# Performance work log

Measured on AMD Instinct MI355X. Metric: run time of the kernel, lower is better.

The kernel has to match this reference:

```python
import jax, jax.numpy as jnp
import numpy as np

B, C, H, W, K = 2, 64, 192, 192, 7
PAD = K // 2
EPS = 1e-6


def _win_idx(L):
    # NATTEN border handling: window is shifted (not zero-padded) to stay in-bounds.
    i = jnp.arange(L)
    start = jnp.clip(i - PAD, 0, L - K)            # [L] window start per query pos
    win = start[:, None] + jnp.arange(K)[None]     # [L,K] absolute key positions
    pb = (K - 1) - (i - start)                     # [L] rpb start index per query pos
    pbi = pb[:, None] + jnp.arange(K)[None]        # [L,K] rpb table indices
    return win, pbi


def setup_inputs() -> dict:
    key = jax.random.key(0)
    ks = jax.random.split(key, 10)
    g = jax.random.normal(ks[0], (B, C, H, W), jnp.float32)
    cd = jax.random.uniform(ks[1], (B, 1, H, W), dtype=jnp.float32)
    dense = jax.random.uniform(ks[2], (B, 1, H, W), dtype=jnp.float32)
    sel = jax.random.uniform(ks[3], (B, 1, H, W)) < 0.05
    sd = jnp.where(sel, dense, 0.0)
    mask = (jax.random.uniform(ks[4], (B, 1, H, W)) < 0.5).astype(jnp.float32)
    ln_w = 1.0 + 0.02 * jax.random.normal(ks[5], (C,), jnp.float32)
    ln_b = 0.02 * jax.random.normal(ks[6], (C,), jnp.float32)
    conv_w = 0.05 * jax.random.normal(ks[7], (2 * C, C + 1), jnp.float32)  # 1x1 conv
    conv_b = 0.02 * jax.random.normal(ks[8], (2 * C,), jnp.float32)
    rpb = 0.02 * jax.random.normal(ks[9], (1, 2 * K - 1, 2 * K - 1), jnp.float32)
    return {"g": g, "cd": cd, "sd": sd, "mask": mask,
            "ln_w": ln_w, "ln_b": ln_b, "conv_w": conv_w, "conv_b": conv_b, "rpb": rpb}


def reference(g, cd, sd, mask, ln_w, ln_b, conv_w, conv_b, rpb):
    # LayerNorm2d: normalize over channel dim per spatial location
    mu = g.mean(axis=1, keepdims=True)
    var = ((g - mu) ** 2).mean(axis=1, keepdims=True)
    gn = (g - mu) * jax.lax.rsqrt(var + EPS)
    gn = gn * ln_w[None, :, None, None] + ln_b[None, :, None, None]

    z = jnp.concatenate([gn, cd], axis=1)                      # [B,C+1,H,W]
    qk = jnp.einsum('bchw,oc->bohw', z, conv_w) + conv_b[None, :, None, None]
    q, k = qk[:, :C], qk[:, C:]
    k = k * mask

    qc = q.transpose(0, 2, 3, 1)                               # [B,H,W,C] single head
    kc = k.transpose(0, 2, 3, 1)
    rwin, rpbi = _win_idx(H)
    cwin, cpbi = _win_idx(W)

    # NATTEN qk + relative position bias over 7x7 neighborhoods
    k_win = kc[:, rwin][:, :, :, cwin]                         # [B,H,K,W,K,C]
    attn = jnp.einsum('bhwc,bhiwjc->bhwij', qc, k_win)         # [B,H,W,K,K]
    bias = rpb[0][rpbi][:, :, cpbi]                            # [H,K,W,K]
    attn = attn + bias.transpose(0, 2, 1, 3)[None]
    a = jax.nn.softmax(attn.reshape(B, H, W, K * K), axis=-1).reshape(B, H, W, K, K)

    # NATTEN av with v = cd (head_dim 1)
    v_win = cd[:, 0][:, rwin][:, :, :, cwin]                   # [B,H,K,W,K]
    cd_out = jnp.einsum('bhwij,bhiwj->bhw', a, v_win)[:, None]  # [B,1,H,W]
    m_win = mask[:, 0][:, rwin][:, :, :, cwin]
    mask_out = jnp.einsum('bhwij,bhiwj->bhw', a, m_win)[:, None]

    # NYU / SDR post-processing
    cd_out = cd_out * mask + cd * (1.0 - mask)
    valid = sd > 0
    cd_out = jnp.where(valid, sd, cd_out)
    mask_out = jnp.where(valid, mask, mask_out)
    return cd_out, mask_out
```

## Files before the change

### kernel.cpp

```cpp
#include <hip/hip_runtime.h>

constexpr int NB = 2;
constexpr int NC = 64;
constexpr int NH = 192;
constexpr int NW = 192;
constexpr int NK = 7;
constexpr int NHW = NH * NW;
constexpr int NPIX = NB * NHW;
constexpr float EPS = 1e-6f;

__global__ __launch_bounds__(256) void qk_gemm(
    const float* __restrict__ g, const float* __restrict__ cd,
    const float* __restrict__ mask,
    const float* __restrict__ ln_w, const float* __restrict__ ln_b,
    const float* __restrict__ conv_w, const float* __restrict__ conv_b,
    float* __restrict__ qbuf, float* __restrict__ kbuf)
{
    __shared__ float Z[65][128];
    __shared__ float WTc[33][128];

    int tid = threadIdx.x;
    int p0 = blockIdx.x * 128;
    int b  = p0 / NHW;
    int hw0 = p0 - b * NHW;

    int px = tid >> 1;
    int hf = tid & 1;
    const float* gp = g + (size_t)(b * NC + hf * 32) * NHW + (hw0 + px);
    float vals[32];
    float s = 0.f, sq = 0.f;
#pragma unroll
    for (int j = 0; j < 32; ++j) {
        float v = gp[(size_t)j * NHW];
        vals[j] = v; s += v; sq += v * v;
    }
    s  += __shfl_xor(s, 1);
    sq += __shfl_xor(sq, 1);
    float mu   = s * (1.f / 64.f);
    float rstd = rsqrtf(sq * (1.f / 64.f) - mu * mu + EPS);
#pragma unroll
    for (int j = 0; j < 32; ++j) {
        int c = hf * 32 + j;
        Z[c][px] = (vals[j] - mu) * rstd * ln_w[c] + ln_b[c];
    }
    if (hf) Z[64][px] = cd[p0 + px];

    int og = tid >> 4;
    int pg = tid & 15;
    float acc[8][8];
#pragma unroll
    for (int oi = 0; oi < 8; ++oi)
#pragma unroll
        for (int pj = 0; pj < 8; ++pj) acc[oi][pj] = 0.f;

    for (int cc = 0; cc < 65; cc += 33) {
        int nr = (65 - cc < 33) ? (65 - cc) : 33;
        __syncthreads();
        if (tid < 128) {
            int o = tid;
            for (int r = 0; r < nr; ++r)
                WTc[r][o] = conv_w[o * 65 + cc + r];
        }
        __syncthreads();
        for (int r = 0; r < nr; ++r) {
            float4 w0 = *(const float4*)&WTc[r][8 * og];
            float4 w1 = *(const float4*)&WTc[r][8 * og + 4];
            float4 z0 = *(const float4*)&Z[cc + r][8 * pg];
            float4 z1 = *(const float4*)&Z[cc + r][8 * pg + 4];
            float w8[8] = {w0.x, w0.y, w0.z, w0.w, w1.x, w1.y, w1.z, w1.w};
            float z8[8] = {z0.x, z0.y, z0.z, z0.w, z1.x, z1.y, z1.z, z1.w};
#pragma unroll
            for (int oi = 0; oi < 8; ++oi)
#pragma unroll
                for (int pj = 0; pj < 8; ++pj)
                    acc[oi][pj] = fmaf(w8[oi], z8[pj], acc[oi][pj]);
        }
    }

    int o0  = og * 8;
    int pxb = pg * 8;
    float4 ba = *(const float4*)&conv_b[o0];
    float4 bb = *(const float4*)&conv_b[o0 + 4];
    float bia[8] = {ba.x, ba.y, ba.z, ba.w, bb.x, bb.y, bb.z, bb.w};
    bool isq = (o0 < 64);
    float m8[8];
    if (!isq) {
        float4 ma = *(const float4*)&mask[p0 + pxb];
        float4 mc = *(const float4*)&mask[p0 + pxb + 4];
        m8[0]=ma.x; m8[1]=ma.y; m8[2]=ma.z; m8[3]=ma.w;
        m8[4]=mc.x; m8[5]=mc.y; m8[6]=mc.z; m8[7]=mc.w;
    }
    float* base = isq ? (qbuf + (size_t)(b * NC + o0) * NHW + hw0 + pxb)
                      : (kbuf + (size_t)(b * NC + o0 - 64) * NHW + hw0 + pxb);
#pragma unroll
    for (int oi = 0; oi < 8; ++oi) {
        float v[8];
#pragma unroll
        for (int pj = 0; pj < 8; ++pj) {
            float t = acc[oi][pj] + bia[oi];
            v[pj] = isq ? t : t * m8[pj];
        }
        float* dst = base + (size_t)oi * NHW;
        *(float4*)&dst[0] = make_float4(v[0], v[1], v[2], v[3]);
        *(float4*)&dst[4] = make_float4(v[4], v[5], v[6], v[7]);
    }
}

__global__ __launch_bounds__(256) void attn_tile(
    const float* __restrict__ qbuf, const float* __restrict__ kbuf,
    const float* __restrict__ cd, const float* __restrict__ sd,
    const float* __restrict__ mask, const float* __restrict__ rpb,
    float* __restrict__ out_cd, float* __restrict__ out_mask)
{
    __shared__ float kst[2][2][22 * 23];
    __shared__ float cdt[22 * 23];
    __shared__ float mt [22 * 23];
    __shared__ float rpbt[169];
    __shared__ float xbuf[128][98];

    int tid  = threadIdx.x;
    int idx  = tid & 127;
    int half = tid >> 7;

    int bw = blockIdx.x % 12;
    int t2 = blockIdx.x / 12;
    int bh = t2 % 12;
    int b  = t2 / 12;
    int w0 = bw * 16, h0 = bh * 16;

    int tx = idx & 7, ty = idx >> 3;
    int h  = h0 + ty;
    int wA = w0 + 2 * tx;
    int rs  = min(max(h - 3, 0), NH - NK);
    int cs0 = min(max(wA - 3, 0), NW - NK);
    int cs1 = min(max(wA - 2, 0), NW - NK);
    int d1  = cs1 - cs0;
    int rb  = (rs - h0 + 3) * 23 + (cs0 - w0 + 3);

    int soff[4], slds[4], sact[4];
#pragma unroll
    for (int sI = 0; sI < 4; ++sI) {
        int e = idx + 128 * sI;
        int r = e / 22, x = e - r * 22;
        int gr = min(max(h0 - 3 + r, 0), NH - 1);
        int gc = min(max(w0 - 3 + x, 0), NW - 1);
        soff[sI] = gr * NW + gc;
        slds[sI] = r * 23 + x;
        sact[sI] = (e < 484);
    }

    const float* cdb = cd   + (size_t)b * NHW;
    const float* msb = mask + (size_t)b * NHW;
    for (int e = tid; e < 484; e += 256) {
        int r = e / 22, x = e - r * 22;
        int gr = min(max(h0 - 3 + r, 0), NH - 1);
        int gc = min(max(w0 - 3 + x, 0), NW - 1);
        cdt[r * 23 + x] = cdb[gr * NW + gc];
        mt [r * 23 + x] = msb[gr * NW + gc];
    }
    if (tid < 169) rpbt[tid] = rpb[tid];

    const float* kb = kbuf + (size_t)(b * NC + half * 32) * NHW;
    const float* qb = qbuf + (size_t)(b * NC + half * 32) * NHW + (h * NW + wA);

    float at0[49], at1[49];
#pragma unroll
    for (int n = 0; n < 49; ++n) { at0[n] = 0.f; at1[n] = 0.f; }

    float st[4];
#pragma unroll
    for (int sI = 0; sI < 4; ++sI)
        st[sI] = sact[sI] ? kb[soff[sI]] : 0.f;
    float* myk0 = kst[half][0];
    float* myk1 = kst[half][1];
#pragma unroll
    for (int sI = 0; sI < 4; ++sI)
        if (sact[sI]) myk0[slds[sI]] = st[sI];

    for (int i = 0; i < 32; ++i) {
        __syncthreads();
        if (i + 1 < 32) {
            const float* kb2 = kb + (size_t)(i + 1) * NHW;
#pragma unroll
            for (int sI = 0; sI < 4; ++sI)
                st[sI] = sact[sI] ? kb2[soff[sI]] : 0.f;
        }
        float2 q2 = *(const float2*)(qb + (size_t)i * NHW);
        const float* kt = ((i & 1) ? myk1 : myk0) + rb;
#pragma unroll
        for (int r = 0; r < 7; ++r) {
            float kr[8];
#pragma unroll
            for (int j = 0; j < 8; ++j) kr[j] = kt[r * 23 + j];
#pragma unroll
            for (int j = 0; j < 7; ++j) {
                float kA = kr[j];
                float kB = d1 ? kr[j + 1] : kr[j];
                at0[r * 7 + j] = fmaf(q2.x, kA, at0[r * 7 + j]);
                at1[r * 7 + j] = fmaf(q2.y, kB, at1[r * 7 + j]);
            }
        }
        if (i + 1 < 32) {
            float* nk = (i & 1) ? myk0 : myk1;
#pragma unroll
            for (int sI = 0; sI < 4; ++sI)
                if (sact[sI]) nk[slds[sI]] = st[sI];
        }
    }

    float* xr = xbuf[idx];
    __syncthreads();
    if (half == 1) {
#pragma unroll
        for (int n = 0; n < 49; ++n)
            *(float2*)&xr[2 * n] = make_float2(at0[n], at1[n]);
    }
    __syncthreads();
    int pr  = 6 - (h - rs);
    int pc0 = 6 - (wA - cs0);
    int pc1 = 6 - (wA + 1 - cs1);
    if (half == 0) {
#pragma unroll
        for (int n = 0; n < 49; ++n) {
            float2 v = *(const float2*)&xr[2 * n];
            at0[n] += v.x; at1[n] += v.y;
        }
#pragma unroll
        for (int r = 0; r < 7; ++r)
#pragma unroll
            for (int j = 0; j < 7; ++j) {
                at0[r * 7 + j] += rpbt[(pr + r) * 13 + pc0 + j];
                at1[r * 7 + j] += rpbt[(pr + r) * 13 + pc1 + j];
            }
#pragma unroll
        for (int n = 0; n < 49; ++n)
            *(float2*)&xr[2 * n] = make_float2(at0[n], at1[n]);
    }
    __syncthreads();
    if (half == 1) {
#pragma unroll
        for (int n = 0; n < 49; ++n) {
            float2 v = *(const float2*)&xr[2 * n];
            at0[n] = v.x; at1[n] = v.y;
        }
    }

    float mx0 = -1e30f, mx1 = -1e30f;
#pragma unroll
    for (int n = 0; n < 49; ++n) {
        mx0 = fmaxf(mx0, at0[n]); mx1 = fmaxf(mx1, at1[n]);
    }
    float sm0 = 0.f, sm1 = 0.f;
#pragma unroll
    for (int n = 0; n < 49; ++n) {
        at0[n] = __expf(at0[n] - mx0); sm0 += at0[n];
        at1[n] = __expf(at1[n] - mx1); sm1 += at1[n];
    }

    const float* vt = half ? mt : cdt;
    float s0 = 0.f, s1 = 0.f;
#pragma unroll
    for (int r = 0; r < 7; ++r) {
        float vr[8];
#pragma unroll
        for (int j = 0; j < 8; ++j) vr[j] = vt[rb + r * 23 + j];
#pragma unroll
        for (int j = 0; j < 7; ++j) {
            float vA = vr[j];
            float vB = d1 ? vr[j + 1] : vr[j];
            s0 = fmaf(at0[r * 7 + j], vA, s0);
            s1 = fmaf(at1[r * 7 + j], vB, s1);
        }
    }
    s0 /= sm0; s1 /= sm1;

    int cidx = (ty + 3) * 23 + (2 * tx + 3);
    float mc0 = mt[cidx], mc1 = mt[cidx + 1];
    int p = b * NHW + h * NW + wA;
    float2 sd2 = *(const float2*)&sd[p];
    if (half == 0) {
        float cdc0 = cdt[cidx], cdc1 = cdt[cidx + 1];
        float c0 = s0 * mc0 + cdc0 * (1.f - mc0);
        float c1 = s1 * mc1 + cdc1 * (1.f - mc1);
        if (sd2.x > 0.f) c0 = sd2.x;
        if (sd2.y > 0.f) c1 = sd2.y;
        *(float2*)&out_cd[p] = make_float2(c0, c1);
    } else {
        float m0 = (sd2.x > 0.f) ? mc0 : s0;
        float m1 = (sd2.y > 0.f) ? mc1 : s1;
        *(float2*)&out_mask[p] = make_float2(m0, m1);
    }
}

extern "C" void kernel_launch(void* const* d_in, const int* in_sizes, int n_in,
                              void* d_out, int out_size, void* d_ws, size_t ws_size,
                              hipStream_t stream) {
    const float* g      = (const float*)d_in[0];
    const float* cd     = (const float*)d_in[1];
    const float* sd     = (const float*)d_in[2];
    const float* mask   = (const float*)d_in[3];
    const float* ln_w   = (const float*)d_in[4];
    const float* ln_b   = (const float*)d_in[5];
    const float* conv_w = (const float*)d_in[6];
    const float* conv_b = (const float*)d_in[7];
    const float* rpb    = (const float*)d_in[8];

    float* out  = (float*)d_out;
    float* qbuf = (float*)d_ws;
    float* kbuf = qbuf + (size_t)NB * NC * NHW;

    qk_gemm<<<dim3(NPIX / 128), dim3(256), 0, stream>>>(
        g, cd, mask, ln_w, ln_b, conv_w, conv_b, qbuf, kbuf);
    attn_tile<<<dim3(NB * 144), dim3(256), 0, stream>>>(
        qbuf, kbuf, cd, sd, mask, rpb, out, out + NPIX);
}
```

Before: 144.9 us.

## Restructure attention tile to one pixel per thread with per-wave K staging

The attention kernel now uses 16x8 tiles split into four 64-thread wave groups. Each group stages its own 10x22 K halo and double-buffers it without block-wide barriers in the channel loop. Each thread now handles one pixel instead of two, so the grid doubles to 576 blocks and the at0/at1 register arrays shrink to a single 49-entry array, which should raise occupancy and fill more CUs. In exchange, halo reloads overlap between the two row-groups, so global K traffic per pixel rises, and each pixel loses the shared K row reuse it had before.

```diff
diff --git a/kernel.cpp b/kernel.cpp
--- a/kernel.cpp
+++ b/kernel.cpp
@@ -112,183 +112,148 @@
     const float* __restrict__ mask, const float* __restrict__ rpb,
     float* __restrict__ out_cd, float* __restrict__ out_mask)
 {
-    __shared__ float kst[2][2][22 * 23];
-    __shared__ float cdt[22 * 23];
-    __shared__ float mt [22 * 23];
+    __shared__ float kst[4][2][10 * 24];
+    __shared__ float cdt[14 * 24];
+    __shared__ float mt [14 * 24];
     __shared__ float rpbt[169];
-    __shared__ float xbuf[128][98];
+    __shared__ float xch[128][49];
 
     int tid  = threadIdx.x;
-    int idx  = tid & 127;
-    int half = tid >> 7;
+    int g    = tid >> 6;
+    int lane = tid & 63;
+    int rq   = g & 1;
+    int half = g >> 1;
+    int tx   = lane & 15;
+    int tyw  = lane >> 4;
 
     int bw = blockIdx.x % 12;
     int t2 = blockIdx.x / 12;
-    int bh = t2 % 12;
-    int b  = t2 / 12;
-    int w0 = bw * 16, h0 = bh * 16;
-
-    int tx = idx & 7, ty = idx >> 3;
-    int h  = h0 + ty;
-    int wA = w0 + 2 * tx;
-    int rs  = min(max(h - 3, 0), NH - NK);
-    int cs0 = min(max(wA - 3, 0), NW - NK);
-    int cs1 = min(max(wA - 2, 0), NW - NK);
-    int d1  = cs1 - cs0;
-    int rb  = (rs - h0 + 3) * 23 + (cs0 - w0 + 3);
-
-    int soff[4], slds[4], sact[4];
-#pragma unroll
-    for (int sI = 0; sI < 4; ++sI) {
-        int e = idx + 128 * sI;
-        int r = e / 22, x = e - r * 22;
-        int gr = min(max(h0 - 3 + r, 0), NH - 1);
-        int gc = min(max(w0 - 3 + x, 0), NW - 1);
-        soff[sI] = gr * NW + gc;
-        slds[sI] = r * 23 + x;
-        sact[sI] = (e < 484);
-    }
+    int bh = t2 % 24;
+    int b  = t2 / 24;
+    int w0 = bw * 16, h0 = bh * 8;
+    int hr0 = h0 + rq * 4;
+
+    int h = hr0 + tyw;
+    int w = w0 + tx;
+    int rs = min(max(h - 3, 0), NH - NK);
+    int cs = min(max(w - 3, 0), NW - NK);
+    int rb  = (rs - (hr0 - 3)) * 24 + (cs - (w0 - 3));
+    int rbB = (rs - (h0  - 3)) * 24 + (cs - (w0 - 3));
 
     const float* cdb = cd   + (size_t)b * NHW;
     const float* msb = mask + (size_t)b * NHW;
-    for (int e = tid; e < 484; e += 256) {
-        int r = e / 22, x = e - r * 22;
+    for (int e = tid; e < 308; e += 256) {
+        int r = e / 22, c2 = e - r * 22;
         int gr = min(max(h0 - 3 + r, 0), NH - 1);
-        int gc = min(max(w0 - 3 + x, 0), NW - 1);
-        cdt[r * 23 + x] = cdb[gr * NW + gc];
-        mt [r * 23 + x] = msb[gr * NW + gc];
+        int gc = min(max(w0 - 3 + c2, 0), NW - 1);
+        cdt[r * 24 + c2] = cdb[gr * NW + gc];
+        mt [r * 24 + c2] = msb[gr * NW + gc];
     }
     if (tid < 169) rpbt[tid] = rpb[tid];
 
+    int soff[4], slds[4]; bool sact[4];
+#pragma unroll
+    for (int s = 0; s < 4; ++s) {
+        int e = lane + 64 * s;
+        int r = e / 22, c2 = e - r * 22;
+        int gr = min(max(hr0 - 3 + r, 0), NH - 1);
+        int gc = min(max(w0 - 3 + c2, 0), NW - 1);
+        soff[s] = gr * NW + gc;
+        slds[s] = r * 24 + c2;
+        sact[s] = (e < 220);
+    }
+
     const float* kb = kbuf + (size_t)(b * NC + half * 32) * NHW;
-    const float* qb = qbuf + (size_t)(b * NC + half * 32) * NHW + (h * NW + wA);
-
-    float at0[49], at1[49];
-#pragma unroll
-    for (int n = 0; n < 49; ++n) { at0[n] = 0.f; at1[n] = 0.f; }
+    const float* qb = qbuf + (size_t)(b * NC + half * 32) * NHW + h * NW + w;
+
+    float at[49];
+#pragma unroll
+    for (int n = 0; n < 49; ++n) at[n] = 0.f;
 
     float st[4];
 #pragma unroll
-    for (int sI = 0; sI < 4; ++sI)
-        st[sI] = sact[sI] ? kb[soff[sI]] : 0.f;
-    float* myk0 = kst[half][0];
-    float* myk1 = kst[half][1];
-#pragma unroll
-    for (int sI = 0; sI < 4; ++sI)
-        if (sact[sI]) myk0[slds[sI]] = st[sI];
+    for (int s = 0; s < 4; ++s) st[s] = sact[s] ? kb[soff[s]] : 0.f;
+    float* k0 = kst[g][0];
+    float* k1 = kst[g][1];
+#pragma unroll
+    for (int s = 0; s < 4; ++s) if (sact[s]) k0[slds[s]] = st[s];
 
     for (int i = 0; i < 32; ++i) {
-        __syncthreads();
         if (i + 1 < 32) {
             const float* kb2 = kb + (size_t)(i + 1) * NHW;
 #pragma unroll
-            for (int sI = 0; sI < 4; ++sI)
-                st[sI] = sact[sI] ? kb2[soff[sI]] : 0.f;
-        }
-        float2 q2 = *(const float2*)(qb + (size_t)i * NHW);
-        const float* kt = ((i & 1) ? myk1 : myk0) + rb;
-#pragma unroll
-        for (int r = 0; r < 7; ++r) {
-            float kr[8];
-#pragma unroll
-            for (int j = 0; j < 8; ++j) kr[j] = kt[r * 23 + j];
-#pragma unroll
-            for (int j = 0; j < 7; ++j) {
-                float kA = kr[j];
-                float kB = d1 ? kr[j + 1] : kr[j];
-                at0[r * 7 + j] = fmaf(q2.x, kA, at0[r * 7 + j]);
-                at1[r * 7 + j] = fmaf(q2.y, kB, at1[r * 7 + j]);
-            }
-        }
+            for (int s = 0; s < 4; ++s) st[s] = sact[s] ? kb2[soff[s]] : 0.f;
+        }
+        float q = qb[(size_t)i * NHW];
+        const float* kt = ((i & 1) ? k1 : k0) + rb;
+#pragma unroll
+        for (int r = 0; r < 7; ++r)
+#pragma unroll
+            for (int j = 0; j < 7; ++j)
+                at[r * 7 + j] = fmaf(q, kt[r * 24 + j], at[r * 7 + j]);
         if (i + 1 < 32) {
-            float* nk = (i & 1) ? myk0 : myk1;
-#pragma unroll
-            for (int sI = 0; sI < 4; ++sI)
-                if (sact[sI]) nk[slds[sI]] = st[sI];
-        }
-    }
-
-    float* xr = xbuf[idx];
+            float* nk = (i & 1) ? k0 : k1;
+#pragma unroll
+            for (int s = 0; s < 4; ++s) if (sact[s]) nk[slds[s]] = st[s];
+        }
+    }
+
+    int pxid = (rq * 4 + tyw) * 16 + tx;
     __syncthreads();
     if (half == 1) {
 #pragma unroll
-        for (int n = 0; n < 49; ++n)
-            *(float2*)&xr[2 * n] = make_float2(at0[n], at1[n]);
+        for (int n = 0; n < 49; ++n) xch[pxid][n] = at[n];
     }
     __syncthreads();
-    int pr  = 6 - (h - rs);
-    int pc0 = 6 - (wA - cs0);
-    int pc1 = 6 - (wA + 1 - cs1);
+    int pr = 6 - (h - rs);
+    int pc = 6 - (w - cs);
     if (half == 0) {
 #pragma unroll
-        for (int n = 0; n < 49; ++n) {
-            float2 v = *(const float2*)&xr[2 * n];
-            at0[n] += v.x; at1[n] += v.y;
-        }
+        for (int n = 0; n < 49; ++n) at[n] += xch[pxid][n];
 #pragma unroll
         for (int r = 0; r < 7; ++r)
 #pragma unroll
-            for (int j = 0; j < 7; ++j) {
-                at0[r * 7 + j] += rpbt[(pr + r) * 13 + pc0 + j];
-                at1[r * 7 + j] += rpbt[(pr + r) * 13 + pc1 + j];
-            }
-#pragma unroll
-        for (int n = 0; n < 49; ++n)
-            *(float2*)&xr[2 * n] = make_float2(at0[n], at1[n]);
+            for (int j = 0; j < 7; ++j)
+                at[r * 7 + j] += rpbt[(pr + r) * 13 + pc + j];
+#pragma unroll
+        for (int n = 0; n < 49; ++n) xch[pxid][n] = at[n];
     }
     __syncthreads();
     if (half == 1) {
 #pragma unroll
-        for (int n = 0; n < 49; ++n) {
-            float2 v = *(const float2*)&xr[2 * n];
-            at0[n] = v.x; at1[n] = v.y;
-        }
-    }
-
-    float mx0 = -1e30f, mx1 = -1e30f;
+        for (int n = 0; n < 49; ++n) at[n] = xch[pxid][n];
+    }
+
+    float mx = -1e30f;
+#pragma unroll
+    for (int n = 0; n < 49; ++n) mx = fmaxf(mx, at[n]);
+    float sm = 0.f;
 #pragma unroll
     for (int n = 0; n < 49; ++n) {
-        mx0 = fmaxf(mx0, at0[n]); mx1 = fmaxf(mx1, at1[n]);
-    }
-    float sm0 = 0.f, sm1 = 0.f;
-#pragma unroll
-    for (int n = 0; n < 49; ++n) {
-        at0[n] = __expf(at0[n] - mx0); sm0 += at0[n];
-        at1[n] = __expf(at1[n] - mx1); sm1 += at1[n];
-    }
-
-    const float* vt = half ? mt : cdt;
-    float s0 = 0.f, s1 = 0.f;
-#pragma unroll
-    for (int r = 0; r < 7; ++r) {
-        float vr[8];
-#pragma unroll
-        for (int j = 0; j < 8; ++j) vr[j] = vt[rb + r * 23 + j];
-#pragma unroll
-        for (int j = 0; j < 7; ++j) {
-            float vA = vr[j];
-            float vB = d1 ? vr[j + 1] : vr[j];
-            s0 = fmaf(at0[r * 7 + j], vA, s0);
-            s1 = fmaf(at1[r * 7 + j], vB, s1);
-        }
-    }
-    s0 /= sm0; s1 /= sm1;
-
-    int cidx = (ty + 3) * 23 + (2 * tx + 3);
-    float mc0 = mt[cidx], mc1 = mt[cidx + 1];
-    int p = b * NHW + h * NW + wA;
-    float2 sd2 = *(const float2*)&sd[p];
+        at[n] = __expf(at[n] - mx);
+        sm += at[n];
+    }
+
+    const float* vt = (half ? mt : cdt) + rbB;
+    float sv = 0.f;
+#pragma unroll
+    for (int r = 0; r < 7; ++r)
+#pragma unroll
+        for (int j = 0; j < 7; ++j)
+            sv = fmaf(at[r * 7 + j], vt[r * 24 + j], sv);
+    sv /= sm;
+
+    int p = b * NHW + h * NW + w;
+    float sdc = sd[p];
+    int cidx = (rq * 4 + tyw + 3) * 24 + (tx + 3);
+    float mc = mt[cidx];
     if (half == 0) {
-        float cdc0 = cdt[cidx], cdc1 = cdt[cidx + 1];
-        float c0 = s0 * mc0 + cdc0 * (1.f - mc0);
-        float c1 = s1 * mc1 + cdc1 * (1.f - mc1);
-        if (sd2.x > 0.f) c0 = sd2.x;
-        if (sd2.y > 0.f) c1 = sd2.y;
-        *(float2*)&out_cd[p] = make_float2(c0, c1);
+        float cdc = cdt[cidx];
+        float co = sv * mc + cdc * (1.f - mc);
+        if (sdc > 0.f) co = sdc;
+        out_cd[p] = co;
     } else {
-        float m0 = (sd2.x > 0.f) ? mc0 : s0;
-        float m1 = (sd2.y > 0.f) ? mc1 : s1;
-        *(float2*)&out_mask[p] = make_float2(m0, m1);
+        out_mask[p] = (sdc > 0.f) ? mc : sv;
     }
 }
 
@@ -311,6 +276,6 @@
 
     qk_gemm<<<dim3(NPIX / 128), dim3(256), 0, stream>>>(
         g, cd, mask, ln_w, ln_b, conv_w, conv_b, qbuf, kbuf);
-    attn_tile<<<dim3(NB * 144), dim3(256), 0, stream>>>(
+    attn_tile<<<dim3(NB * 24 * 12), dim3(256), 0, stream>>>(
         qbuf, kbuf, cd, sd, mask, rpb, out, out + NPIX);
 }
```

Result: faster. 140.7 us (-2.9%).
